# Kernel tuning notes

Hardware: AMD Instinct MI355X
Metric: run time of the kernel (lower is better)

Reference implementation:

```python
import jax, jax.numpy as jnp
import numpy as np

D_MODEL = 1024
HEADS = 16
D_K = D_MODEL // HEADS
D_FF = 4096
B, S = 4, 2048
EPS = 1e-5


def _layer_norm(x, gamma, beta):
    mu = jnp.mean(x, axis=-1, keepdims=True)
    var = jnp.mean(jnp.square(x - mu), axis=-1, keepdims=True)
    return (x - mu) * jax.lax.rsqrt(var + EPS) * gamma + beta


def setup_inputs() -> dict:
    key = jax.random.key(0)
    ks = jax.random.split(key, 16)
    s_in = 1.0 / np.sqrt(D_MODEL)
    s_ff = 1.0 / np.sqrt(D_FF)
    inp = {
        "x": jax.random.normal(ks[0], (B, S, D_MODEL), dtype=jnp.float32),
        "src_mask": jnp.ones((B, 1, 1, S), dtype=jnp.int32),
        "Wq": jax.random.uniform(ks[1], (D_MODEL, D_MODEL), jnp.float32, -s_in, s_in),
        "bq": jnp.zeros((D_MODEL,), jnp.float32),
        "Wk": jax.random.uniform(ks[2], (D_MODEL, D_MODEL), jnp.float32, -s_in, s_in),
        "bk": jnp.zeros((D_MODEL,), jnp.float32),
        "Wv": jax.random.uniform(ks[3], (D_MODEL, D_MODEL), jnp.float32, -s_in, s_in),
        "bv": jnp.zeros((D_MODEL,), jnp.float32),
        "Wo": jax.random.uniform(ks[4], (D_MODEL, D_MODEL), jnp.float32, -s_in, s_in),
        "bo": jnp.zeros((D_MODEL,), jnp.float32),
        "W1": jax.random.uniform(ks[5], (D_MODEL, D_FF), jnp.float32, -s_in, s_in),
        "b1": jnp.zeros((D_FF,), jnp.float32),
        "W2": jax.random.uniform(ks[6], (D_FF, D_MODEL), jnp.float32, -s_ff, s_ff),
        "b2": jnp.zeros((D_MODEL,), jnp.float32),
        "g1": jnp.ones((D_MODEL,), jnp.float32),
        "be1": jnp.zeros((D_MODEL,), jnp.float32),
        "g2": jnp.ones((D_MODEL,), jnp.float32),
        "be2": jnp.zeros((D_MODEL,), jnp.float32),
    }
    return inp


def reference(x, src_mask, Wq, bq, Wk, bk, Wv, bv, Wo, bo, W1, b1, W2, b2, g1, be1, g2, be2):
    Bn, L, _ = x.shape
    # Self-attention (dropout=0 / eval)
    q = (x @ Wq + bq).reshape(Bn, L, HEADS, D_K).transpose(0, 2, 1, 3)  # [B,H,L,dk]
    k = (x @ Wk + bk).reshape(Bn, L, HEADS, D_K).transpose(0, 2, 1, 3)
    v = (x @ Wv + bv).reshape(Bn, L, HEADS, D_K).transpose(0, 2, 1, 3)
    scores = jnp.einsum("bhqd,bhkd->bhqk", q, k) / np.sqrt(D_K).astype(np.float32)
    scores = jnp.where(src_mask == 0, -jnp.inf, scores)
    attn = jax.nn.softmax(scores, axis=-1)
    out = jnp.einsum("bhqk,bhkd->bhqd", attn, v)
    out = out.transpose(0, 2, 1, 3).reshape(Bn, L, D_MODEL)
    attn_out = out @ Wo + bo
    x = _layer_norm(x + attn_out, g1, be1)
    # FFN
    ffn = jax.nn.relu(x @ W1 + b1) @ W2 + b2
    x = _layer_norm(x + ffn, g2, be2)
    return x
```

## Files before the change

### kernel.cpp

```cpp
#include <hip/hip_runtime.h>
#include <hip/hip_bf16.h>
#include <cstdint>
#include <cstddef>

typedef __bf16 bf16;
typedef __bf16 bf16x8 __attribute__((ext_vector_type(8)));
typedef float  f32x4  __attribute__((ext_vector_type(4)));
typedef unsigned short u16x4 __attribute__((ext_vector_type(4)));
typedef uint32_t u32x4 __attribute__((ext_vector_type(4)));

static constexpr int D_MODEL = 1024;
static constexpr int HEADS   = 16;
static constexpr int D_KH    = 64;
static constexpr int D_FF    = 4096;
static constexpr int BATCH   = 4;
static constexpr int SEQ     = 2048;
static constexpr int MROWS   = BATCH * SEQ;

#define VMCNT(n) asm volatile("s_waitcnt vmcnt(" #n ")" ::: "memory")
#define LGKM0()                                            \
  do {                                                     \
    asm volatile("s_waitcnt lgkmcnt(0)" ::: "memory");     \
    __builtin_amdgcn_sched_barrier(0);                     \
  } while (0)

__device__ __forceinline__ unsigned short bfbits(float f) {
  return __builtin_bit_cast(unsigned short, (bf16)f);
}

__device__ __forceinline__ void gload_lds16(const void* g, void* l) {
  __builtin_amdgcn_global_load_lds(
      (__attribute__((address_space(1))) uint32_t*)(uintptr_t)g,
      (__attribute__((address_space(3))) uint32_t*)(uintptr_t)l, 16, 0, 0);
}

__global__ void k_cast_bf16(const float* __restrict__ in, bf16* __restrict__ out) {
  int i = (blockIdx.x * 256 + threadIdx.x) * 8;
  const float4* p = (const float4*)(in + i);
  float4 a = p[0], b = p[1];
  bf16x8 v;
  v[0] = (bf16)a.x; v[1] = (bf16)a.y; v[2] = (bf16)a.z; v[3] = (bf16)a.w;
  v[4] = (bf16)b.x; v[5] = (bf16)b.y; v[6] = (bf16)b.z; v[7] = (bf16)b.w;
  *(bf16x8*)(out + i) = v;
}

struct TP4 { const float* src[4]; bf16* dst[4]; };
__global__ void k_transpose_cast4(TP4 p) {
  __shared__ float tile[64][65];
  const float* W = p.src[blockIdx.z];
  bf16* Wt = p.dst[blockIdx.z];
  int k0 = blockIdx.x * 64, n0 = blockIdx.y * 64;
  int c = threadIdx.x & 63, r0 = threadIdx.x >> 6;
#pragma unroll
  for (int i = 0; i < 16; ++i) {
    int r = r0 + i * 4;
    tile[r][c] = W[(size_t)(k0 + r) * 1024 + n0 + c];
  }
  __syncthreads();
#pragma unroll
  for (int i = 0; i < 16; ++i) {
    int r = r0 + i * 4;
    Wt[(size_t)(n0 + r) * 1024 + k0 + c] = (bf16)tile[c][r];
  }
}

__global__ void k_transpose_cast(const float* __restrict__ W, bf16* __restrict__ Wt,
                                 int K, int N) {
  __shared__ float tile[64][65];
  int k0 = blockIdx.x * 64, n0 = blockIdx.y * 64;
  int c = threadIdx.x & 63, r0 = threadIdx.x >> 6;
#pragma unroll
  for (int i = 0; i < 16; ++i) {
    int r = r0 + i * 4;
    tile[r][c] = W[(size_t)(k0 + r) * N + n0 + c];
  }
  __syncthreads();
#pragma unroll
  for (int i = 0; i < 16; ++i) {
    int r = r0 + i * 4;
    Wt[(size_t)(n0 + r) * K + k0 + c] = (bf16)tile[c][r];
  }
}

enum { EP_RELU = 0, EP_F32 = 1, EP_QKV = 2 };

template <int EPI, int NREP>
__global__ __launch_bounds__(512, 2) void k_gemm8(
    const bf16* __restrict__ A, const bf16* __restrict__ Bt,
    const float* __restrict__ bias, const float* __restrict__ bias2,
    const float* __restrict__ bias3,
    void* __restrict__ Cout, void* __restrict__ C2, void* __restrict__ C3,
    int N, int K) {
  extern __shared__ char smem[];
  constexpr int BN = NREP * 64;
  constexpr int HB = NREP / 2;
  const int tid = threadIdx.x;
  const int lane = tid & 63;
  const int wid = tid >> 6;
  const int wm = wid >> 2, wn = wid & 3;
  const int l15 = lane & 15, l4 = lane >> 4;
  const int bx = blockIdx.x, by = blockIdx.y;
  const int NI = K >> 7;

  const int c0 = tid, c1 = tid + 512;
  const bf16* baseA0 = A + (size_t)(bx * 256 + (c0 >> 3)) * K + ((c0 & 7) ^ ((c0 >> 3) & 7)) * 8;
  const bf16* baseA1 = A + (size_t)(bx * 256 + (c1 >> 3)) * K + ((c1 & 7) ^ ((c1 >> 3) & 7)) * 8;
  const bf16* baseB0 = Bt + (size_t)(by * BN + (c0 >> 3)) * K + ((c0 & 7) ^ ((c0 >> 3) & 7)) * 8;
  const bf16* baseB1 = Bt + (size_t)(by * BN + (c1 >> 3)) * K + ((c1 & 7) ^ ((c1 >> 3) & 7)) * 8;
  const size_t rowK128 = (size_t)128 * K;

  auto stA = [&](int h, int t, int buf) {
    gload_lds16(baseA0 + h * rowK128 + t * 64, smem + buf * 32768 + h * 16384 + c0 * 16);
    gload_lds16(baseA1 + h * rowK128 + t * 64, smem + buf * 32768 + h * 16384 + c1 * 16);
  };
  auto stB = [&](int h, int t, int buf) {
    gload_lds16(baseB0 + h * rowK128 + t * 64,
                smem + 65536 + buf * (HB * 16384) + h * 16384 + c0 * 16);
    gload_lds16(baseB1 + h * rowK128 + t * 64,
                smem + 65536 + buf * (HB * 16384) + h * 16384 + c1 * 16);
  };

  const int ch0 = (l4 ^ (l15 & 7)) * 16;
  const int ch1 = ((4 + l4) ^ (l15 & 7)) * 16;
  const int aoff = l15 * 128;
  int boffh[NREP];
#pragma unroll
  for (int n = 0; n < NREP; ++n) {
    int rB = wn * (NREP * 16) + n * 16 + l15;
    boffh[n] = (rB >> 7) * 16384 + (rB & 127) * 128;
  }

  f32x4 acc[8][NREP] = {};
  bf16x8 breg[NREP][2];

  stA(0, 0, 0); stA(1, 0, 0); stB(0, 0, 0);
  if constexpr (HB == 2) stB(1, 0, 0);
  stA(0, 1, 1); stA(1, 1, 1); stB(0, 1, 1);
  if constexpr (HB == 2) stB(1, 1, 1);

  for (int i = 0; i < NI; ++i) {
    const int t1 = 2 * i + 1, t2 = 2 * i + 2;
    const bool notfirst = (i > 0), notlast = (i + 1 < NI);
#pragma unroll
    for (int p = 0; p < 8; ++p) {
      const int q = p & 3;
      const char* Ab = smem + (p >> 2) * 32768 + wm * 16384;
      const char* Bb = smem + 65536 + (p >> 2) * (HB * 16384);
      if (p == 0) {
        if (notfirst) {
          stA(0, t1, 1);
          VMCNT(2);
        } else {
          if constexpr (HB == 2) VMCNT(8); else VMCNT(6);
        }
        __builtin_amdgcn_s_barrier();
      } else if (p == 4) {
        if (notlast) {
          stA(0, t2, 0);
          VMCNT(2);
        } else {
          VMCNT(0);
        }
        __builtin_amdgcn_s_barrier();
      }
      if (q == 0) {
#pragma unroll
        for (int n = 0; n < NREP; ++n) {
          breg[n][0] = *(const bf16x8*)(Bb + boffh[n] + ch0);
          breg[n][1] = *(const bf16x8*)(Bb + boffh[n] + ch1);
        }
      }
      bf16x8 a0k0 = *(const bf16x8*)(Ab + (2 * q + 0) * 2048 + aoff + ch0);
      bf16x8 a0k1 = *(const bf16x8*)(Ab + (2 * q + 0) * 2048 + aoff + ch1);
      bf16x8 a1k0 = *(const bf16x8*)(Ab + (2 * q + 1) * 2048 + aoff + ch0);
      bf16x8 a1k1 = *(const bf16x8*)(Ab + (2 * q + 1) * 2048 + aoff + ch1);
      if (p == 1) { if (notfirst) stA(1, t1, 1); }
      else if (p == 2) { if (notfirst) stB(0, t1, 1); }
      else if (p == 3) { if constexpr (HB == 2) { if (notfirst) stB(1, t1, 1); } }
      else if (p == 5) { if (notlast) stA(1, t2, 0); }
      else if (p == 6) { if (notlast) stB(0, t2, 0); }
      else if (p == 7) { if constexpr (HB == 2) { if (notlast) stB(1, t2, 0); } }
      if (p != 0 && p != 4) __builtin_amdgcn_s_barrier();
      LGKM0();
      __builtin_amdgcn_s_setprio(1);
#pragma unroll
      for (int n = 0; n < NREP; ++n) {
        acc[2 * q + 0][n] = __builtin_amdgcn_mfma_f32_16x16x32_bf16(a0k0, breg[n][0], acc[2 * q + 0][n], 0, 0, 0);
        acc[2 * q + 0][n] = __builtin_amdgcn_mfma_f32_16x16x32_bf16(a0k1, breg[n][1], acc[2 * q + 0][n], 0, 0, 0);
        acc[2 * q + 1][n] = __builtin_amdgcn_mfma_f32_16x16x32_bf16(a1k0, breg[n][0], acc[2 * q + 1][n], 0, 0, 0);
        acc[2 * q + 1][n] = __builtin_amdgcn_mfma_f32_16x16x32_bf16(a1k1, breg[n][1], acc[2 * q + 1][n], 0, 0, 0);
      }
      __builtin_amdgcn_s_setprio(0);
      __builtin_amdgcn_s_barrier();
    }
  }

  float bia[NREP];
#pragma unroll
  for (int n = 0; n < NREP; ++n) {
    int colL = wn * (NREP * 16) + n * 16 + l15;
    if constexpr (EPI == EP_QKV) {
      const int g = by >> 2;
      const float* bp = (g == 0) ? bias : (g == 1 ? bias2 : bias3);
      bia[n] = bp[(by & 3) * 256 + colL];
    } else {
      bia[n] = bias[by * BN + colL];
    }
  }
#pragma unroll
  for (int mf = 0; mf < 8; ++mf) {
    int row0 = bx * 256 + wm * 128 + mf * 16 + l4 * 4;
#pragma unroll
    for (int n = 0; n < NREP; ++n) {
      int colL = wn * (NREP * 16) + n * 16 + l15;
      if constexpr (EPI == EP_QKV) {
        const int g = by >> 2;
        int cc = (by & 3) * 256 + colL;
        if (g == 2) {
          int bidx = row0 >> 11, s0 = row0 & 2047;
          u16x4 pk;
#pragma unroll
          for (int r = 0; r < 4; ++r) pk[r] = bfbits(acc[mf][n][r] + bia[n]);
          *(u16x4*)((bf16*)C3 + (((size_t)bidx * HEADS + (cc >> 6)) * D_KH + (cc & 63)) * SEQ + s0) = pk;
        } else {
          bf16* dst = g ? (bf16*)C2 : (bf16*)Cout;
#pragma unroll
          for (int r = 0; r < 4; ++r)
            dst[(size_t)(row0 + r) * 1024 + cc] = (bf16)(acc[mf][n][r] + bia[n]);
        }
      } else {
        int col = by * BN + colL;
#pragma unroll
        for (int r = 0; r < 4; ++r) {
          float v = acc[mf][n][r] + bia[n];
          if constexpr (EPI == EP_RELU)
            ((bf16*)Cout)[(size_t)(row0 + r) * N + col] = (bf16)fmaxf(v, 0.f);
          else
            ((float*)Cout)[(size_t)(row0 + r) * N + col] = v;
        }
      }
    }
  }
}

__global__ __launch_bounds__(256, 4) void k_attn(
    const bf16* __restrict__ Q, const bf16* __restrict__ Kb,
    const bf16* __restrict__ Vt, const int* __restrict__ mask,
    bf16* __restrict__ O) {
  __shared__ bf16 Ks[2][64 * 64];
  __shared__ bf16 Vs[2][64 * 64];
  const int tid = threadIdx.x;
  const int lane = tid & 63;
  const int l15 = lane & 15, l4 = lane >> 4;
  const int bh = blockIdx.y, b = bh >> 4, h = bh & 15;
  const size_t qrow0 = (size_t)b * SEQ + blockIdx.x * 128 + (tid >> 6) * 32;
  const bf16* Kbase = Kb + (size_t)b * SEQ * D_MODEL + h * 64;
  const bf16* Vbase = Vt + (size_t)bh * D_KH * SEQ;
  const int* mbase = mask + b * SEQ;
  constexpr float C = 0.18033688011f;

  bf16x8 qf[2][2];
#pragma unroll
  for (int m = 0; m < 2; ++m)
#pragma unroll
    for (int ks = 0; ks < 2; ++ks)
      qf[m][ks] = *(const bf16x8*)&Q[(qrow0 + m * 16 + l15) * D_MODEL + h * 64 + ks * 32 + l4 * 8];

  f32x4 o[2][4] = {};
  float lrun[2] = {0.f, 0.f};

  auto stage = [&](int buf, int kv0) {
#pragma unroll
    for (int i = 0; i < 2; ++i) {
      int o_ = tid + i * 256;
      int row = o_ >> 3;
      int ch = (o_ & 7) ^ (row & 7);
      gload_lds16(Kbase + (size_t)(kv0 + row) * D_MODEL + ch * 8,
                  (char*)&Ks[buf][0] + o_ * 16);
      gload_lds16(Vbase + (size_t)row * SEQ + kv0 + ch * 8,
                  (char*)&Vs[buf][0] + o_ * 16);
    }
  };

  stage(0, 0);
  __syncthreads();

  const int sl0 = l15 + (((2 * l4) & 3) << 4);
  const int sl1 = l15 + (((2 * l4 + 1) & 3) << 4);
  const bool hiSel = l4 >= 2;

  for (int kv0 = 0; kv0 < SEQ; kv0 += 64) {
    const int cur = (kv0 >> 6) & 1;
    if (kv0 + 64 < SEQ) stage(cur ^ 1, kv0 + 64);
    const bf16* Kc = &Ks[cur][0];
    const bf16* Vc = &Vs[cur][0];

    f32x4 sf[2][4] = {};
    __builtin_amdgcn_s_setprio(1);
#pragma unroll
    for (int ks = 0; ks < 2; ++ks)
#pragma unroll
      for (int n = 0; n < 4; ++n) {
        int r = n * 16 + l15;
        bf16x8 kf = *(const bf16x8*)&Kc[r * 64 + ((ks * 32 + l4 * 8) ^ ((r & 7) << 3))];
#pragma unroll
        for (int m = 0; m < 2; ++m)
          sf[m][n] = __builtin_amdgcn_mfma_f32_16x16x32_bf16(kf, qf[m][ks], sf[m][n], 0, 0, 0);
      }
    __builtin_amdgcn_s_setprio(0);

    int4 mk[4];
#pragma unroll
    for (int n = 0; n < 4; ++n)
      mk[n] = *(const int4*)&mbase[kv0 + n * 16 + l4 * 4];
    int allm = 1;
#pragma unroll
    for (int n = 0; n < 4; ++n)
      allm &= (mk[n].x & mk[n].y & mk[n].z & mk[n].w);
    if (__builtin_expect(!__all(allm != 0), 0)) {
#pragma unroll
      for (int n = 0; n < 4; ++n)
#pragma unroll
        for (int r = 0; r < 4; ++r)
          if (((const int*)&mk[n])[r] == 0) {
            sf[0][n][r] = -1e30f;
            sf[1][n][r] = -1e30f;
          }
    }

    uint32_t pk[2][4][2];
#pragma unroll
    for (int m = 0; m < 2; ++m) {
      float ps = 0.f;
#pragma unroll
      for (int n = 0; n < 4; ++n) {
#pragma unroll
        for (int r = 0; r < 4; ++r) {
          float pv = exp2f(sf[m][n][r] * C);
          sf[m][n][r] = pv;
          ps += pv;
        }
        asm("v_cvt_pk_bf16_f32 %0, %1, %2"
            : "=v"(pk[m][n][0]) : "v"(sf[m][n][0]), "v"(sf[m][n][1]));
        asm("v_cvt_pk_bf16_f32 %0, %1, %2"
            : "=v"(pk[m][n][1]) : "v"(sf[m][n][2]), "v"(sf[m][n][3]));
      }
      lrun[m] += ps;
    }

    bf16x8 pa[2][2];
#pragma unroll
    for (int ks = 0; ks < 2; ++ks)
#pragma unroll
      for (int m = 0; m < 2; ++m) {
        u32x4 w;
#pragma unroll
        for (int wi = 0; wi < 4; ++wi) {
          int sl = (wi & 2) ? sl1 : sl0;
          uint32_t va = (uint32_t)__shfl((int)pk[m][ks * 2 + 0][wi & 1], sl);
          uint32_t vb = (uint32_t)__shfl((int)pk[m][ks * 2 + 1][wi & 1], sl);
          w[wi] = hiSel ? vb : va;
        }
        pa[ks][m] = __builtin_bit_cast(bf16x8, w);
      }

#pragma unroll
    for (int ks = 0; ks < 2; ++ks) {
      __builtin_amdgcn_s_setprio(1);
#pragma unroll
      for (int n = 0; n < 4; ++n) {
        int d = n * 16 + l15;
        bf16x8 vf = *(const bf16x8*)&Vc[d * 64 + ((ks * 32 + l4 * 8) ^ ((d & 7) << 3))];
#pragma unroll
        for (int m = 0; m < 2; ++m)
          o[m][n] = __builtin_amdgcn_mfma_f32_16x16x32_bf16(pa[ks][m], vf, o[m][n], 0, 0, 0);
      }
      __builtin_amdgcn_s_setprio(0);
    }
    __syncthreads();
  }

#pragma unroll
  for (int m = 0; m < 2; ++m) {
    lrun[m] += __shfl_xor(lrun[m], 16);
    lrun[m] += __shfl_xor(lrun[m], 32);
  }
#pragma unroll
  for (int m = 0; m < 2; ++m) {
    float inv[4];
#pragma unroll
    for (int r = 0; r < 4; ++r)
      inv[r] = 1.0f / __shfl(lrun[m], l4 * 4 + r);
#pragma unroll
    for (int n = 0; n < 4; ++n)
#pragma unroll
      for (int r = 0; r < 4; ++r)
        O[(qrow0 + m * 16 + l4 * 4 + r) * D_MODEL + h * 64 + n * 16 + l15] =
            (bf16)(o[m][n][r] * inv[r]);
  }
}

__global__ __launch_bounds__(256) void k_add_ln(
    const float* __restrict__ a, const float* __restrict__ b,
    const float* __restrict__ g, const float* __restrict__ be,
    float* __restrict__ yf, bf16* __restrict__ yb) {
  const int t = threadIdx.x;
  const size_t base = (size_t)blockIdx.x * D_MODEL + t * 4;
  float4 va = *(const float4*)(a + base);
  float4 vb = *(const float4*)(b + base);
  float v0 = va.x + vb.x, v1 = va.y + vb.y, v2 = va.z + vb.z, v3 = va.w + vb.w;
  float s  = v0 + v1 + v2 + v3;
  float s2 = v0 * v0 + v1 * v1 + v2 * v2 + v3 * v3;
#pragma unroll
  for (int off = 1; off < 64; off <<= 1) {
    s  += __shfl_xor(s, off);
    s2 += __shfl_xor(s2, off);
  }
  __shared__ float red1[4], red2[4];
  int w = t >> 6;
  if ((t & 63) == 0) { red1[w] = s; red2[w] = s2; }
  __syncthreads();
  s  = red1[0] + red1[1] + red1[2] + red1[3];
  s2 = red2[0] + red2[1] + red2[2] + red2[3];
  float mu  = s * (1.f / D_MODEL);
  float var = s2 * (1.f / D_MODEL) - mu * mu;
  float rstd = rsqrtf(var + 1e-5f);
  float4 vg  = *(const float4*)(g + t * 4);
  float4 vbe = *(const float4*)(be + t * 4);
  float y0 = (v0 - mu) * rstd * vg.x + vbe.x;
  float y1 = (v1 - mu) * rstd * vg.y + vbe.y;
  float y2 = (v2 - mu) * rstd * vg.z + vbe.z;
  float y3 = (v3 - mu) * rstd * vg.w + vbe.w;
  *(float4*)(yf + base) = make_float4(y0, y1, y2, y3);
  if (yb) {
    u16x4 pk = {bfbits(y0), bfbits(y1), bfbits(y2), bfbits(y3)};
    *(u16x4*)(yb + base) = pk;
  }
}

extern "C" void kernel_launch(void* const* d_in, const int* in_sizes, int n_in,
                              void* d_out, int out_size, void* d_ws, size_t ws_size,
                              hipStream_t stream) {
  const float* x   = (const float*)d_in[0];
  const int*  mask = (const int*)d_in[1];
  const float* Wq  = (const float*)d_in[2];
  const float* bq  = (const float*)d_in[3];
  const float* Wk  = (const float*)d_in[4];
  const float* bk_ = (const float*)d_in[5];
  const float* Wv  = (const float*)d_in[6];
  const float* bv  = (const float*)d_in[7];
  const float* Wo  = (const float*)d_in[8];
  const float* bo  = (const float*)d_in[9];
  const float* W1  = (const float*)d_in[10];
  const float* b1  = (const float*)d_in[11];
  const float* W2  = (const float*)d_in[12];
  const float* b2  = (const float*)d_in[13];
  const float* g1  = (const float*)d_in[14];
  const float* be1 = (const float*)d_in[15];
  const float* g2  = (const float*)d_in[16];
  const float* be2 = (const float*)d_in[17];

  char* ws = (char*)d_ws;
  const size_t MB = 1ull << 20;
  bf16*  xb   = (bf16*)(ws + 0);
  bf16*  Qb   = (bf16*)(ws + 16 * MB);
  bf16*  Kbuf = (bf16*)(ws + 32 * MB);
  bf16*  Vt   = (bf16*)(ws + 48 * MB);
  bf16*  Hb   = (bf16*)(ws + 0);
  float* f32a = (float*)(ws + 64 * MB);
  float* x1f  = (float*)(ws + 96 * MB);
  bf16*  x1b  = (bf16*)(ws + 128 * MB);
  bf16*  Wqkvt= (bf16*)(ws + 144 * MB);
  bf16*  Wot  = (bf16*)(ws + 150 * MB);
  bf16*  W1t  = (bf16*)(ws + 152 * MB);
  bf16*  W2t  = (bf16*)(ws + 160 * MB);
  bf16*  Ob   = xb;

  const int SM4 = 131072, SM2 = 98304;
  hipFuncSetAttribute(reinterpret_cast<const void*>(&k_gemm8<EP_QKV, 4>),
                      hipFuncAttributeMaxDynamicSharedMemorySize, SM4);
  hipFuncSetAttribute(reinterpret_cast<const void*>(&k_gemm8<EP_RELU, 4>),
                      hipFuncAttributeMaxDynamicSharedMemorySize, SM4);
  hipFuncSetAttribute(reinterpret_cast<const void*>(&k_gemm8<EP_F32, 2>),
                      hipFuncAttributeMaxDynamicSharedMemorySize, SM2);

  k_cast_bf16<<<MROWS * D_MODEL / (256 * 8), 256, 0, stream>>>(x, xb);
  TP4 tp;
  tp.src[0] = Wq; tp.dst[0] = Wqkvt;
  tp.src[1] = Wk; tp.dst[1] = Wqkvt + 1024 * 1024;
  tp.src[2] = Wv; tp.dst[2] = Wqkvt + 2 * 1024 * 1024;
  tp.src[3] = Wo; tp.dst[3] = Wot;
  k_transpose_cast4<<<dim3(16, 16, 4), 256, 0, stream>>>(tp);
  k_transpose_cast<<<dim3(16, 64), 256, 0, stream>>>(W1, W1t, 1024, 4096);
  k_transpose_cast<<<dim3(64, 16), 256, 0, stream>>>(W2, W2t, 4096, 1024);

  k_gemm8<EP_QKV, 4><<<dim3(32, 12), 512, SM4, stream>>>(
      xb, Wqkvt, bq, bk_, bv, Qb, Kbuf, Vt, 3072, 1024);

  k_attn<<<dim3(16, 64), 256, 0, stream>>>(Qb, Kbuf, Vt, mask, Ob);

  k_gemm8<EP_F32, 2><<<dim3(32, 8), 512, SM2, stream>>>(
      Ob, Wot, bo, nullptr, nullptr, f32a, nullptr, nullptr, 1024, 1024);
  k_add_ln<<<MROWS, 256, 0, stream>>>(x, f32a, g1, be1, x1f, x1b);

  k_gemm8<EP_RELU, 4><<<dim3(32, 16), 512, SM4, stream>>>(
      x1b, W1t, b1, nullptr, nullptr, Hb, nullptr, nullptr, 4096, 1024);
  k_gemm8<EP_F32, 2><<<dim3(32, 8), 512, SM2, stream>>>(
      Hb, W2t, b2, nullptr, nullptr, f32a, nullptr, nullptr, 1024, 4096);
  k_add_ln<<<MROWS, 256, 0, stream>>>(x1f, f32a, g2, be2, (float*)d_out, nullptr);
}
```

Baseline: 402.5 us.

## Precompute mask tile flags, remap attention blocks per XCD, use permlane swaps

Adds a tiny kernel that computes a per-batch bitmask marking which 64-key tiles are fully unmasked, so the attention loop no longer loads and reduces mask values on every tile. The attention grid is flattened and remapped so that blocks sharing the same batch-head land on the same XCD, which is meant to improve L2 reuse of K/V. The P-fragment reshuffle switches from ds_bpermute shuffles to v_permlane32/16_swap instructions. This adds an extra small launch and a workspace slot for the flags.

```diff
diff --git a/kernel.cpp b/kernel.cpp
--- a/kernel.cpp
+++ b/kernel.cpp
@@ -42,6 +42,24 @@
   v[0] = (bf16)a.x; v[1] = (bf16)a.y; v[2] = (bf16)a.z; v[3] = (bf16)a.w;
   v[4] = (bf16)b.x; v[5] = (bf16)b.y; v[6] = (bf16)b.z; v[7] = (bf16)b.w;
   *(bf16x8*)(out + i) = v;
+}
+
+__global__ void k_mask_flags(const int* __restrict__ mask, uint32_t* __restrict__ flags) {
+  __shared__ uint32_t sb[4];
+  int tid = threadIdx.x;
+  if (tid < 4) sb[tid] = 0;
+  __syncthreads();
+  int b = tid >> 5, t = tid & 31;
+  const int4* p = (const int4*)(mask + b * SEQ + t * 64);
+  int all = 1;
+#pragma unroll
+  for (int i = 0; i < 16; ++i) {
+    int4 v = p[i];
+    all &= v.x & v.y & v.z & v.w;
+  }
+  if (all) atomicOr(&sb[b], 1u << t);
+  __syncthreads();
+  if (tid < 4) flags[tid] = sb[tid];
 }
 
 struct TP4 { const float* src[4]; bf16* dst[4]; };
@@ -246,17 +264,22 @@
 __global__ __launch_bounds__(256, 4) void k_attn(
     const bf16* __restrict__ Q, const bf16* __restrict__ Kb,
     const bf16* __restrict__ Vt, const int* __restrict__ mask,
-    bf16* __restrict__ O) {
+    const uint32_t* __restrict__ Mf, bf16* __restrict__ O) {
   __shared__ bf16 Ks[2][64 * 64];
   __shared__ bf16 Vs[2][64 * 64];
   const int tid = threadIdx.x;
   const int lane = tid & 63;
   const int l15 = lane & 15, l4 = lane >> 4;
-  const int bh = blockIdx.y, b = bh >> 4, h = bh & 15;
-  const size_t qrow0 = (size_t)b * SEQ + blockIdx.x * 128 + (tid >> 6) * 32;
+  const int L = blockIdx.x;
+  const int xcd = L & 7, rest = L >> 3;
+  const int qx = rest & 15, yhi = rest >> 4;
+  const int bh = yhi * 8 + xcd;
+  const int b = bh >> 4, h = bh & 15;
+  const size_t qrow0 = (size_t)b * SEQ + qx * 128 + (tid >> 6) * 32;
   const bf16* Kbase = Kb + (size_t)b * SEQ * D_MODEL + h * 64;
   const bf16* Vbase = Vt + (size_t)bh * D_KH * SEQ;
   const int* mbase = mask + b * SEQ;
+  const uint32_t mflags = Mf[b];
   constexpr float C = 0.18033688011f;
 
   bf16x8 qf[2][2];
@@ -285,10 +308,6 @@
   stage(0, 0);
   __syncthreads();
 
-  const int sl0 = l15 + (((2 * l4) & 3) << 4);
-  const int sl1 = l15 + (((2 * l4 + 1) & 3) << 4);
-  const bool hiSel = l4 >= 2;
-
   for (int kv0 = 0; kv0 < SEQ; kv0 += 64) {
     const int cur = (kv0 >> 6) & 1;
     if (kv0 + 64 < SEQ) stage(cur ^ 1, kv0 + 64);
@@ -309,23 +328,17 @@
       }
     __builtin_amdgcn_s_setprio(0);
 
-    int4 mk[4];
-#pragma unroll
-    for (int n = 0; n < 4; ++n)
-      mk[n] = *(const int4*)&mbase[kv0 + n * 16 + l4 * 4];
-    int allm = 1;
-#pragma unroll
-    for (int n = 0; n < 4; ++n)
-      allm &= (mk[n].x & mk[n].y & mk[n].z & mk[n].w);
-    if (__builtin_expect(!__all(allm != 0), 0)) {
-#pragma unroll
-      for (int n = 0; n < 4; ++n)
+    if (__builtin_expect(!((mflags >> (kv0 >> 6)) & 1), 0)) {
+#pragma unroll
+      for (int n = 0; n < 4; ++n) {
+        int4 mk = *(const int4*)&mbase[kv0 + n * 16 + l4 * 4];
 #pragma unroll
         for (int r = 0; r < 4; ++r)
-          if (((const int*)&mk[n])[r] == 0) {
+          if (((const int*)&mk)[r] == 0) {
             sf[0][n][r] = -1e30f;
             sf[1][n][r] = -1e30f;
           }
+      }
     }
 
     uint32_t pk[2][4][2];
@@ -350,16 +363,18 @@
 
     bf16x8 pa[2][2];
 #pragma unroll
-    for (int ks = 0; ks < 2; ++ks)
-#pragma unroll
-      for (int m = 0; m < 2; ++m) {
+    for (int m = 0; m < 2; ++m)
+#pragma unroll
+      for (int ks = 0; ks < 2; ++ks) {
         u32x4 w;
 #pragma unroll
-        for (int wi = 0; wi < 4; ++wi) {
-          int sl = (wi & 2) ? sl1 : sl0;
-          uint32_t va = (uint32_t)__shfl((int)pk[m][ks * 2 + 0][wi & 1], sl);
-          uint32_t vb = (uint32_t)__shfl((int)pk[m][ks * 2 + 1][wi & 1], sl);
-          w[wi] = hiSel ? vb : va;
+        for (int hh = 0; hh < 2; ++hh) {
+          uint32_t a = pk[m][ks * 2 + 0][hh];
+          uint32_t bsw = pk[m][ks * 2 + 1][hh];
+          asm("v_permlane32_swap_b32 %0, %1" : "+v"(a), "+v"(bsw));
+          asm("v_permlane16_swap_b32 %0, %1" : "+v"(a), "+v"(bsw));
+          w[hh] = a;
+          w[2 + hh] = bsw;
         }
         pa[ks][m] = __builtin_bit_cast(bf16x8, w);
       }
@@ -474,6 +489,7 @@
   bf16*  Wot  = (bf16*)(ws + 150 * MB);
   bf16*  W1t  = (bf16*)(ws + 152 * MB);
   bf16*  W2t  = (bf16*)(ws + 160 * MB);
+  uint32_t* mfl = (uint32_t*)(ws + 64 * MB);
   bf16*  Ob   = xb;
 
   const int SM4 = 131072, SM2 = 98304;
@@ -485,6 +501,7 @@
                       hipFuncAttributeMaxDynamicSharedMemorySize, SM2);
 
   k_cast_bf16<<<MROWS * D_MODEL / (256 * 8), 256, 0, stream>>>(x, xb);
+  k_mask_flags<<<1, 128, 0, stream>>>(mask, mfl);
   TP4 tp;
   tp.src[0] = Wq; tp.dst[0] = Wqkvt;
   tp.src[1] = Wk; tp.dst[1] = Wqkvt + 1024 * 1024;
@@ -497,7 +514,7 @@
   k_gemm8<EP_QKV, 4><<<dim3(32, 12), 512, SM4, stream>>>(
       xb, Wqkvt, bq, bk_, bv, Qb, Kbuf, Vt, 3072, 1024);
 
-  k_attn<<<dim3(16, 64), 256, 0, stream>>>(Qb, Kbuf, Vt, mask, Ob);
+  k_attn<<<1024, 256, 0, stream>>>(Qb, Kbuf, Vt, mask, mfl, Ob);
 
   k_gemm8<EP_F32, 2><<<dim3(32, 8), 512, SM2, stream>>>(
       Ob, Wot, bo, nullptr, nullptr, f32a, nullptr, nullptr, 1024, 1024);
```

Result: faster. 387.4 us (-3.7%).
